# Kernel tuning notes

Measured on AMD Instinct MI355X. Metric: run time of the kernel, lower is better.

Reference implementation:

```python
import jax, jax.numpy as jnp
import numpy as np

NUM_HEADS = 8
NEG_INF = -1e9

def setup_inputs() -> dict:
    key = jax.random.key(0)
    k1, k2 = jax.random.split(key)
    B, S, D = 2, 4096, 512
    inputs = jax.random.normal(k1, (B, S, D), dtype=jnp.float32)
    # glorot-style scale for the fused QKV weight
    qkv_weights = jax.random.normal(k2, (D, 3 * D), dtype=jnp.float32) * (1.0 / np.sqrt(D))
    return {"inputs": inputs, "qkv_weights": qkv_weights}

def reference(inputs, qkv_weights):
    B, S, D = inputs.shape
    H = NUM_HEADS
    d = D // H  # head dim
    qkv = jnp.einsum('bsd,de->bse', inputs, qkv_weights)  # (B,S,3D)
    q, k, v = jnp.split(qkv, 3, axis=-1)
    # (B,S,D) -> (B,H,S,d)
    def split_heads(x):
        return x.reshape(B, S, H, d).transpose(0, 2, 1, 3)
    q, k, v = split_heads(q), split_heads(k), split_heads(v)
    scores = jnp.einsum('bhid,bhjd->bhij', q, k) / jnp.sqrt(jnp.asarray(d, inputs.dtype))
    # causal mask as in source: tril * scores + (-1e9) * upper-triangle
    tril = jnp.tril(jnp.ones((S, S), dtype=inputs.dtype))
    scores = tril * scores + NEG_INF * (1.0 - tril)
    a = jax.nn.softmax(scores, axis=-1)
    out = jnp.einsum('bhij,bhjd->bhid', a, v)  # (B,H,S,d)
    return out.transpose(0, 2, 1, 3).reshape(B, S, D)
```

## Files before the change

### kernel.cpp

```cpp
#include <hip/hip_runtime.h>

typedef unsigned short u16;
typedef __bf16 b16;
typedef b16 b16x8 __attribute__((ext_vector_type(8)));
typedef float f32x4 __attribute__((ext_vector_type(4)));
typedef u16 u16x4 __attribute__((ext_vector_type(4)));
typedef u16 u16x8 __attribute__((ext_vector_type(8)));
typedef float f4 __attribute__((ext_vector_type(4)));

#define NH 8
#define SEQ 4096
#define DM 512
#define HDIM 64
#define GM 8192
#define GK 512
#define GN 1536

#define QSCALE 0.18033688011112042f
#define SMBIAS 14.0f

__device__ __forceinline__ u16 f2bf(float f) {
  b16 h = (b16)f;
  return __builtin_bit_cast(u16, h);
}

__device__ __forceinline__ void gl16(const u16* g, u16* l) {
  __builtin_amdgcn_global_load_lds((const __attribute__((address_space(1))) void*)g,
                                   (__attribute__((address_space(3))) void*)l, 16, 0, 0);
}

__global__ __launch_bounds__(256) void cvt_fused(const float* __restrict__ x,
                                                 u16* __restrict__ y,
                                                 const float* __restrict__ w,
                                                 u16* __restrict__ wt) {
  __shared__ float tile[32][33];
  int bid = blockIdx.x;
  int t = threadIdx.x;
  if (bid < 2048) {
    int i = (bid * 256 + t) * 8;
    f4 a = *(const f4*)(x + i);
    f4 b = *(const f4*)(x + i + 4);
    u16x8 o;
    o[0] = f2bf(a[0]); o[1] = f2bf(a[1]); o[2] = f2bf(a[2]); o[3] = f2bf(a[3]);
    o[4] = f2bf(b[0]); o[5] = f2bf(b[1]); o[6] = f2bf(b[2]); o[7] = f2bf(b[3]);
    *(u16x8*)(y + i) = o;
  } else {
    int q = bid - 2048;
    int n0 = (q % 48) * 32;
    int k0 = (q / 48) * 32;
    int tn = t & 31, tk = t >> 5;
#pragma unroll
    for (int p = 0; p < 4; ++p) {
      int k = tk + p * 8;
      tile[k][tn] = w[(k0 + k) * GN + n0 + tn];
    }
    __syncthreads();
    int n_l = t >> 3, kg = (t & 7) * 4;
    u16x4 o;
#pragma unroll
    for (int i2 = 0; i2 < 4; ++i2) o[i2] = f2bf(tile[kg + i2][n_l]);
    *(u16x4*)(wt + (n0 + n_l) * GK + k0 + kg) = o;
  }
}

__global__ __launch_bounds__(256, 3) void qkv_gemm(const u16* __restrict__ A,
                                                   const u16* __restrict__ Wt,
                                                   u16* __restrict__ Q,
                                                   u16* __restrict__ K,
                                                   u16* __restrict__ V) {
  __shared__ __align__(16) u16 As[3][4096];
  __shared__ __align__(16) u16 Bs[3][4096];
  int bm = blockIdx.x * 128;
  int bn = blockIdx.y * 128;
  int t = threadIdx.x;
  int lane = t & 63, w = t >> 6;
  int wr = w >> 1, wc = w & 1;
  int l15 = lane & 15, g = lane >> 4;

  f32x4 acc[4][4];
#pragma unroll
  for (int i = 0; i < 4; ++i)
#pragma unroll
    for (int j = 0; j < 4; ++j) {
      acc[i][j][0] = 0.f; acc[i][j][1] = 0.f; acc[i][j][2] = 0.f; acc[i][j][3] = 0.f;
    }

#define GSTAGE(slot, k0) do {                                                   \
    _Pragma("unroll")                                                           \
    for (int p = 0; p < 2; ++p) {                                               \
      int cid = p * 256 + t;                                                    \
      int row = cid >> 2, co = (cid & 3) * 8;                                   \
      gl16(A + (size_t)(bm + row) * GK + (k0) + co, &As[slot][cid * 8]);        \
      gl16(Wt + (size_t)(bn + row) * GK + (k0) + co, &Bs[slot][cid * 8]);       \
    }                                                                           \
  } while (0)

  GSTAGE(0, 0);
  GSTAGE(1, 32);
  int cur = 0;
  for (int kk = 0; kk < 16; ++kk) {
    asm volatile("s_waitcnt vmcnt(4)" ::: "memory");
    __builtin_amdgcn_s_barrier();
    int pk = kk + 2 < 16 ? kk + 2 : 15;
    int slot = cur + 2; if (slot >= 3) slot -= 3;
    GSTAGE(slot, pk * 32);

    b16x8 af[4], bf[4];
#pragma unroll
    for (int mi = 0; mi < 4; ++mi)
      af[mi] = *(const b16x8*)(&As[cur][(wr * 64 + mi * 16 + l15) * 32 + g * 8]);
#pragma unroll
    for (int ni = 0; ni < 4; ++ni)
      bf[ni] = *(const b16x8*)(&Bs[cur][(wc * 64 + ni * 16 + l15) * 32 + g * 8]);
    __builtin_amdgcn_s_setprio(1);
#pragma unroll
    for (int mi = 0; mi < 4; ++mi)
#pragma unroll
      for (int ni = 0; ni < 4; ++ni)
        acc[mi][ni] = __builtin_amdgcn_mfma_f32_16x16x32_bf16(af[mi], bf[ni], acc[mi][ni], 0, 0, 0);
    __builtin_amdgcn_s_setprio(0);
    cur = (cur == 2) ? 0 : cur + 1;
  }

#pragma unroll
  for (int mi = 0; mi < 4; ++mi)
#pragma unroll
    for (int ni = 0; ni < 4; ++ni) {
      int e = bn + wc * 64 + ni * 16 + l15;
      int which = e >> 9, col = e & 511;
      int h = col >> 6, dd = col & 63;
      u16* dst = which == 0 ? Q : (which == 1 ? K : V);
      float scale = (which == 0) ? QSCALE : 1.0f;
#pragma unroll
      for (int r = 0; r < 4; ++r) {
        int m = bm + wr * 64 + mi * 16 + g * 4 + r;
        int b = m >> 12, s = m & 4095;
        dst[(((b * NH + h) * SEQ) + s) * HDIM + dd] = f2bf(acc[mi][ni][r] * scale);
      }
    }
}

__global__ __launch_bounds__(256) void transpose_v(const u16* __restrict__ V,
                                                   u16* __restrict__ Vt) {
  __shared__ u16 tl[64][72];
  int bh = blockIdx.x >> 6;
  int s0 = (blockIdx.x & 63) * 64;
  const u16* src = V + ((size_t)bh * SEQ + s0) * HDIM;
  u16* dst = Vt + (size_t)bh * HDIM * SEQ + s0;
  int t = threadIdx.x;
#pragma unroll
  for (int p = 0; p < 2; ++p) {
    int cid = p * 256 + t;
    int row = cid >> 3, ch = cid & 7;
    *(u16x8*)(&tl[row][ch * 8]) = *(const u16x8*)(src + row * HDIM + ch * 8);
  }
  __syncthreads();
#pragma unroll
  for (int p = 0; p < 4; ++p) {
    int cid = p * 256 + t;
    int dd = cid >> 4, idx = cid & 15;
    int c = idx >> 2, g = idx & 3;
    int base = (c >> 1) * 32 + g * 8 + (c & 1) * 4;
    u16x4 o;
#pragma unroll
    for (int r = 0; r < 4; ++r) o[r] = tl[c * 16 + g * 4 + r][dd];
    *(u16x4*)(dst + dd * SEQ + base) = o;
  }
}

__global__ __launch_bounds__(256, 4) void attn(const u16* __restrict__ Q,
                                               const u16* __restrict__ Kv,
                                               const u16* __restrict__ Vtg,
                                               float* __restrict__ out) {
  int id = blockIdx.x;
  int bh = id & 15;
  int i = id >> 4;
  int j = i & 15, pp = i >> 4;
  int qt = (pp == 0) ? 63 - j : (pp == 1) ? j : (pp == 2) ? 47 - j : 16 + j;
  int b = bh >> 3, h = bh & 7;
  const u16* Qb = Q + (size_t)bh * SEQ * HDIM;
  const u16* Kb = Kv + (size_t)bh * SEQ * HDIM;
  const u16* Vb = Vtg + (size_t)bh * HDIM * SEQ;
  int t = threadIdx.x, lane = t & 63, w = t >> 6;
  int l15 = lane & 15, g = lane >> 4;
  int qb = qt * 64;
  int qw = qb + w * 16;

  __shared__ __align__(16) u16 Ks[2][4096];
  __shared__ __align__(16) u16 Vs[3][4096];

  int rsub = lane >> 3, cp = lane & 7;
  int ch = cp ^ rsub;
  int xorp = (l15 & 7) << 3;

  b16x8 qf[2];
#pragma unroll
  for (int ks = 0; ks < 2; ++ks)
    qf[ks] = *(const b16x8*)(Qb + (qw + l15) * HDIM + ks * 32 + g * 8);

  b16x8 vone;
#pragma unroll
  for (int ii = 0; ii < 8; ++ii) vone[ii] = __builtin_bit_cast(b16, (u16)0x3F80);

  f32x4 oaccT[4], lacc;
#pragma unroll
  for (int ii = 0; ii < 4; ++ii) {
    oaccT[ii][0] = 0.f; oaccT[ii][1] = 0.f; oaccT[ii][2] = 0.f; oaccT[ii][3] = 0.f;
    lacc[ii] = 0.f;
  }
  b16x8 ptp[2];

#define STAGE2(kslot, vslot, jj) do {                                           \
    _Pragma("unroll")                                                           \
    for (int p = 0; p < 2; ++p) {                                               \
      int row = (w * 2 + p) * 8 + rsub;                                         \
      gl16(Kb + (size_t)((jj) + row) * HDIM + ch * 8, &Ks[kslot][(w * 2 + p) * 512]); \
      gl16(Vb + (size_t)row * SEQ + (jj) + ch * 8, &Vs[vslot][(w * 2 + p) * 512]);   \
    }                                                                           \
  } while (0)

#define QKT(st, kslot) do {                                                     \
    _Pragma("unroll")                                                           \
    for (int c = 0; c < 4; ++c) {                                               \
      st[c][0] = -SMBIAS; st[c][1] = -SMBIAS; st[c][2] = -SMBIAS; st[c][3] = -SMBIAS; \
    }                                                                           \
    _Pragma("unroll")                                                           \
    for (int c = 0; c < 4; ++c) {                                               \
      const u16* kr = Ks[kslot] + (c * 16 + l15) * 64;                          \
      b16x8 kf0 = *(const b16x8*)(kr + ((g * 8) ^ xorp));                       \
      b16x8 kf1 = *(const b16x8*)(kr + ((32 + g * 8) ^ xorp));                  \
      st[c] = __builtin_amdgcn_mfma_f32_16x16x32_bf16(kf0, qf[0], st[c], 0, 0, 0); \
      st[c] = __builtin_amdgcn_mfma_f32_16x16x32_bf16(kf1, qf[1], st[c], 0, 0, 0); \
    }                                                                           \
  } while (0)

#define SMREG(st, jj, ptX) do {                                                 \
    if ((jj) + 63 > qw) {                                                       \
      int qq = qw + l15;                                                        \
      _Pragma("unroll")                                                         \
      for (int c = 0; c < 4; ++c)                                               \
        _Pragma("unroll")                                                       \
        for (int r = 0; r < 4; ++r) {                                           \
          int kvg = (jj) + c * 16 + g * 4 + r;                                  \
          if (kvg > qq) st[c][r] = -1e30f;                                      \
        }                                                                       \
    }                                                                           \
    _Pragma("unroll")                                                           \
    for (int c = 0; c < 4; ++c)                                                 \
      _Pragma("unroll")                                                         \
      for (int r = 0; r < 4; ++r)                                               \
        ptX[c >> 1][(c & 1) * 4 + r] = (b16)__builtin_amdgcn_exp2f(st[c][r]);   \
  } while (0)

  int nt = qt + 1;

  STAGE2(0, 0, 0);
  asm volatile("s_waitcnt vmcnt(0)" ::: "memory");
  __builtin_amdgcn_s_barrier();
  if (nt > 1) STAGE2(1, 1, 64);
  {
    f32x4 s0[4];
    QKT(s0, 0);
    SMREG(s0, 0, ptp);
  }

  for (int tt = 0; tt < nt; ++tt) {
    asm volatile("s_waitcnt vmcnt(0)" ::: "memory");
    __builtin_amdgcn_s_barrier();

    if (tt + 2 < nt) STAGE2(tt & 1, (tt + 2) % 3, (tt + 2) * 64);

    bool more = (tt + 1 < nt);
    f32x4 st[4];
    __builtin_amdgcn_s_setprio(1);
    if (more) QKT(st, (tt + 1) & 1);

    const u16* Vc = Vs[tt % 3];
#pragma unroll
    for (int ks = 0; ks < 2; ++ks) {
      int eoff = (ks * 32 + g * 8);
      lacc = __builtin_amdgcn_mfma_f32_16x16x32_bf16(vone, ptp[ks], lacc, 0, 0, 0);
#pragma unroll
      for (int tdd = 0; tdd < 4; ++tdd) {
        b16x8 vf = *(const b16x8*)(Vc + (tdd * 16 + l15) * 64 + (eoff ^ xorp));
        oaccT[tdd] = __builtin_amdgcn_mfma_f32_16x16x32_bf16(vf, ptp[ks], oaccT[tdd], 0, 0, 0);
      }
    }
    __builtin_amdgcn_s_setprio(0);

    if (more) SMREG(st, (tt + 1) * 64, ptp);
  }

  float inv = 1.0f / lacc[0];
  size_t rowbase = ((size_t)b * SEQ + qw + l15) * DM + h * HDIM;
#pragma unroll
  for (int tdd = 0; tdd < 4; ++tdd)
#pragma unroll
    for (int r = 0; r < 4; ++r)
      out[rowbase + tdd * 16 + g * 4 + r] = oaccT[tdd][r] * inv;
}

extern "C" void kernel_launch(void* const* d_in, const int* in_sizes, int n_in,
                              void* d_out, int out_size, void* d_ws, size_t ws_size,
                              hipStream_t stream) {
  const float* x = (const float*)d_in[0];
  const float* wq = (const float*)d_in[1];
  float* out = (float*)d_out;
  char* ws = (char*)d_ws;

  u16* A  = (u16*)ws;
  u16* Wt = (u16*)(ws + 8388608);
  u16* Qw = (u16*)(ws + 8388608 + 1572864);
  u16* Kw = Qw + 4194304;
  u16* Vw = Kw + 4194304;
  u16* Vt = A;

  cvt_fused<<<2816, 256, 0, stream>>>(x, A, wq, Wt);
  dim3 gg(64, 12);
  qkv_gemm<<<gg, 256, 0, stream>>>(A, Wt, Qw, Kw, Vw);
  transpose_v<<<1024, 256, 0, stream>>>(Vw, Vt);
  attn<<<1024, 256, 0, stream>>>(Qw, Kw, Vt, out);
}
```

Before: 88.89 us.

## Fuse V transpose into QKV GEMM epilogue and relax attention prefetch waits

The GEMM epilogue now stages the output tile in shared memory and writes Q/K as 16-byte coalesced rows. The V tile is written directly in the transposed, permuted layout that attention expects, so the separate transpose_v kernel and its launch and round trip through memory go away. In attention, K loads are issued before V loads and the loop waits with vmcnt(2) instead of vmcnt(0), with a prefetch issued every iteration (clamped to the last tile) to keep the counter arithmetic consistent. This lets the V loads of the latest prefetch stay in flight while computing, at the cost of redundant reloads near the end of the loop and a tricky wait-count invariant.

```diff
diff --git a/kernel.cpp b/kernel.cpp
--- a/kernel.cpp
+++ b/kernel.cpp
@@ -67,7 +67,7 @@
                                                    const u16* __restrict__ Wt,
                                                    u16* __restrict__ Q,
                                                    u16* __restrict__ K,
-                                                   u16* __restrict__ V) {
+                                                   u16* __restrict__ Vt) {
   __shared__ __align__(16) u16 As[3][4096];
   __shared__ __align__(16) u16 Bs[3][4096];
   int bm = blockIdx.x * 128;
@@ -122,49 +122,60 @@
     cur = (cur == 2) ? 0 : cur + 1;
   }
 
-#pragma unroll
-  for (int mi = 0; mi < 4; ++mi)
-#pragma unroll
-    for (int ni = 0; ni < 4; ++ni) {
-      int e = bn + wc * 64 + ni * 16 + l15;
-      int which = e >> 9, col = e & 511;
-      int h = col >> 6, dd = col & 63;
-      u16* dst = which == 0 ? Q : (which == 1 ? K : V);
-      float scale = (which == 0) ? QSCALE : 1.0f;
-#pragma unroll
-      for (int r = 0; r < 4; ++r) {
-        int m = bm + wr * 64 + mi * 16 + g * 4 + r;
-        int b = m >> 12, s = m & 4095;
-        dst[(((b * NH + h) * SEQ) + s) * HDIM + dd] = f2bf(acc[mi][ni][r] * scale);
+  __syncthreads();
+  u16* eps = As[0];
+  const int LDE = 132;
+  int which = bn >> 9;
+  int h0 = (bn & 511) >> 6;
+
+  if (which < 2) {
+    float scale = (which == 0) ? QSCALE : 1.0f;
+#pragma unroll
+    for (int mi = 0; mi < 4; ++mi)
+#pragma unroll
+      for (int ni = 0; ni < 4; ++ni) {
+        int e_l = wc * 64 + ni * 16 + l15;
+#pragma unroll
+        for (int r = 0; r < 4; ++r) {
+          int m = wr * 64 + mi * 16 + g * 4 + r;
+          eps[m * LDE + e_l] = f2bf(acc[mi][ni][r] * scale);
+        }
       }
-    }
-}
-
-__global__ __launch_bounds__(256) void transpose_v(const u16* __restrict__ V,
-                                                   u16* __restrict__ Vt) {
-  __shared__ u16 tl[64][72];
-  int bh = blockIdx.x >> 6;
-  int s0 = (blockIdx.x & 63) * 64;
-  const u16* src = V + ((size_t)bh * SEQ + s0) * HDIM;
-  u16* dst = Vt + (size_t)bh * HDIM * SEQ + s0;
-  int t = threadIdx.x;
-#pragma unroll
-  for (int p = 0; p < 2; ++p) {
-    int cid = p * 256 + t;
-    int row = cid >> 3, ch = cid & 7;
-    *(u16x8*)(&tl[row][ch * 8]) = *(const u16x8*)(src + row * HDIM + ch * 8);
-  }
-  __syncthreads();
-#pragma unroll
-  for (int p = 0; p < 4; ++p) {
-    int cid = p * 256 + t;
-    int dd = cid >> 4, idx = cid & 15;
-    int c = idx >> 2, g = idx & 3;
-    int base = (c >> 1) * 32 + g * 8 + (c & 1) * 4;
-    u16x4 o;
-#pragma unroll
-    for (int r = 0; r < 4; ++r) o[r] = tl[c * 16 + g * 4 + r][dd];
-    *(u16x4*)(dst + dd * SEQ + base) = o;
+    __syncthreads();
+    u16* dst = (which == 0) ? Q : K;
+#pragma unroll
+    for (int pass = 0; pass < 8; ++pass) {
+      int hh = pass & 1;
+      int mrow = (pass >> 1) * 32 + (t >> 3);
+      int chunk = t & 7;
+      u16x8 v = *(const u16x8*)(eps + mrow * LDE + hh * 64 + chunk * 8);
+      int mg = bm + mrow;
+      int b = mg >> 12, s = mg & 4095;
+      *(u16x8*)(dst + ((size_t)((b * NH + h0 + hh) * SEQ) + s) * HDIM + chunk * 8) = v;
+    }
+  } else {
+#pragma unroll
+    for (int mi = 0; mi < 4; ++mi)
+#pragma unroll
+      for (int ni = 0; ni < 4; ++ni) {
+        int e_l = wc * 64 + ni * 16 + l15;
+#pragma unroll
+        for (int r = 0; r < 4; ++r) {
+          int m = wr * 64 + mi * 16 + g * 4 + r;
+          int pm = (m & 96) | (((m >> 2) & 3) << 3) | (((m >> 4) & 1) << 2) | (m & 3);
+          eps[e_l * LDE + pm] = f2bf(acc[mi][ni][r]);
+        }
+      }
+    __syncthreads();
+#pragma unroll
+    for (int pass = 0; pass < 8; ++pass) {
+      int rowj = pass * 16 + (t >> 4);
+      int chunk = t & 15;
+      u16x8 v = *(const u16x8*)(eps + rowj * LDE + chunk * 8);
+      int dd = rowj & 63, h = h0 + (rowj >> 6);
+      int b = bm >> 12, s0 = bm & 4095;
+      *(u16x8*)(Vt + ((size_t)((b * NH + h) * HDIM) + dd) * SEQ + s0 + chunk * 8) = v;
+    }
   }
 }
 
@@ -215,6 +226,10 @@
     for (int p = 0; p < 2; ++p) {                                               \
       int row = (w * 2 + p) * 8 + rsub;                                         \
       gl16(Kb + (size_t)((jj) + row) * HDIM + ch * 8, &Ks[kslot][(w * 2 + p) * 512]); \
+    }                                                                           \
+    _Pragma("unroll")                                                           \
+    for (int p = 0; p < 2; ++p) {                                               \
+      int row = (w * 2 + p) * 8 + rsub;                                         \
       gl16(Vb + (size_t)row * SEQ + (jj) + ch * 8, &Vs[vslot][(w * 2 + p) * 512]);   \
     }                                                                           \
   } while (0)
@@ -265,10 +280,15 @@
   }
 
   for (int tt = 0; tt < nt; ++tt) {
-    asm volatile("s_waitcnt vmcnt(0)" ::: "memory");
+    if (nt > 1) {
+      asm volatile("s_waitcnt vmcnt(2)" ::: "memory");
+    } else {
+      asm volatile("s_waitcnt vmcnt(0)" ::: "memory");
+    }
     __builtin_amdgcn_s_barrier();
 
-    if (tt + 2 < nt) STAGE2(tt & 1, (tt + 2) % 3, (tt + 2) * 64);
+    int pft = tt + 2 < nt ? tt + 2 : nt - 1;
+    STAGE2(pft & 1, pft % 3, pft * 64);
 
     bool more = (tt + 1 < nt);
     f32x4 st[4];
@@ -312,12 +332,10 @@
   u16* Wt = (u16*)(ws + 8388608);
   u16* Qw = (u16*)(ws + 8388608 + 1572864);
   u16* Kw = Qw + 4194304;
-  u16* Vw = Kw + 4194304;
-  u16* Vt = A;
+  u16* Vt = Kw + 4194304;
 
   cvt_fused<<<2816, 256, 0, stream>>>(x, A, wq, Wt);
   dim3 gg(64, 12);
-  qkv_gemm<<<gg, 256, 0, stream>>>(A, Wt, Qw, Kw, Vw);
-  transpose_v<<<1024, 256, 0, stream>>>(Vw, Vt);
+  qkv_gemm<<<gg, 256, 0, stream>>>(A, Wt, Qw, Kw, Vt);
   attn<<<1024, 256, 0, stream>>>(Qw, Kw, Vt, out);
 }
```

Measured after the change: 93.04 us. 1.05x slower.
